# Optimization experiments

Hardware: AMD Instinct MI355X
Metric: run time of the kernel (lower is better)

Reference implementation:

```python
import jax, jax.numpy as jnp
import numpy as np

B, D, P, IEXT, T, H = 512, 64, 16, 8, 500, 128
DT = 1.0


def setup_inputs() -> dict:
    key = jax.random.key(0)
    ks = jax.random.split(key, 9)
    s = 0.01  # mimics normal(0.01) kernel init
    return {
        "x": jax.random.normal(ks[0], (B, D, T), jnp.float32),
        "p": jax.random.normal(ks[1], (B, P, T), jnp.float32),
        "i_ext": jax.random.normal(ks[2], (B, IEXT, T), jnp.float32),
        "W0": jax.random.normal(ks[3], (D + P, H), jnp.float32) * s,
        "b0": jax.random.normal(ks[4], (H,), jnp.float32) * s,
        "W1": jax.random.normal(ks[5], (H, H), jnp.float32) * s,
        "b1": jax.random.normal(ks[6], (H,), jnp.float32) * s,
        "W2": jax.random.normal(ks[7], (H, D), jnp.float32) * s,
        "b2": jax.random.normal(ks[8], (D,), jnp.float32) * s,
    }


def reference(x, p, i_ext, W0, b0, W1, b1, W2, b2):
    # Simple_MLP with extra_p=True: concat(state, p) -> Dense+tanh x2 -> Dense
    def mlp(z):
        z = jnp.tanh(z @ W0 + b0)
        z = jnp.tanh(z @ W1 + b1)
        return z @ W2 + b2

    def dfun(state, p_t):
        return mlp(jnp.concatenate([state, p_t], axis=-1))  # [B, D]

    # Heun step: predictor + corrector (two MLP evals), dt = 1.0
    def step(c, p_t):
        d1 = dfun(c, p_t)
        xi = c + DT * d1
        d2 = dfun(xi, p_t)
        nx = c + DT * 0.5 * (d1 + d2)
        return nx, c  # carry new state, emit previous state (as in Heun_step)

    x0 = x[..., 0]                    # [B, D] initial state
    p_seq = jnp.moveaxis(p, 2, 0)     # [T, B, P]
    # i_ext is scanned by the original module but never used by Simple_MLP.
    _, ys = jax.lax.scan(step, x0, p_seq)  # ys: [T, B, D]
    return jnp.moveaxis(ys, 0, 2)     # [B, D, T]
```

## Files before the change

### kernel.cpp

```cpp
#include <hip/hip_runtime.h>

namespace {

constexpr int kB = 512, kD = 64, kP = 16, kT = 500, kH = 128;
constexpr int kRows = 16;
constexpr int kBlocks = kB / kRows;
constexpr int kThreads = 256;

typedef __attribute__((ext_vector_type(8))) short short8;
typedef __attribute__((ext_vector_type(4))) float float4v;
typedef __attribute__((ext_vector_type(2))) unsigned int uint2v;

__device__ __forceinline__ float bf2f(unsigned short u) {
  union { unsigned int i; float f; } v;
  v.i = ((unsigned int)u) << 16;
  return v.f;
}
__device__ __forceinline__ unsigned short f2bf(float f) {
  union { float f; unsigned int i; } v;
  v.f = f;
  return (unsigned short)((v.i + 0x7FFFu + ((v.i >> 16) & 1u)) >> 16);
}
__device__ __forceinline__ void split_bf(float x, unsigned short& hi, unsigned short& lo) {
  hi = f2bf(x);
  lo = f2bf(x - bf2f(hi));
}
#if __has_builtin(__builtin_amdgcn_cvt_pk_bf16_f32)
__device__ __forceinline__ unsigned int pk_bf16(float a, float b) {
  auto v = __builtin_amdgcn_cvt_pk_bf16_f32(a, b);
  unsigned int u;
  __builtin_memcpy(&u, &v, 4);
  return u;
}
#else
__device__ __forceinline__ unsigned int pk_bf16(float a, float b) {
  return (unsigned int)f2bf(a) | ((unsigned int)f2bf(b) << 16);
}
#endif
__device__ __forceinline__ void sp2(float a, float b, unsigned int& hw, unsigned int& lw) {
  unsigned int uh = pk_bf16(a, b);
  float ah, bh;
  { unsigned int t1 = uh << 16; __builtin_memcpy(&ah, &t1, 4); }
  { unsigned int t2 = uh & 0xFFFF0000u; __builtin_memcpy(&bh, &t2, 4); }
  hw = uh;
  lw = pk_bf16(a - ah, b - bh);
}
__device__ __forceinline__ short8 mk8(unsigned int a, unsigned int b, unsigned int c,
                                      unsigned int d) {
  union { unsigned int w[4]; short8 s; } u;
  u.w[0] = a; u.w[1] = b; u.w[2] = c; u.w[3] = d;
  return u.s;
}
__device__ __forceinline__ float fast_tanh(float x) {
  float e = __builtin_amdgcn_exp2f(x * 2.885390081777927f);
  return 1.0f - 2.0f * __builtin_amdgcn_rcpf(e + 1.0f);
}

#define MFMA(a, b, c) __builtin_amdgcn_mfma_f32_16x16x32_bf16((a), (b), (c), 0, 0, 0)

__global__ __launch_bounds__(kThreads, 1) void node_kernel(
    const float* __restrict__ xg, const float* __restrict__ pg,
    const float* __restrict__ w0g, const float* __restrict__ b0g,
    const float* __restrict__ w1g, const float* __restrict__ b1g,
    const float* __restrict__ w2g, const float* __restrict__ b2g,
    float* __restrict__ outg) {
  __shared__ __align__(16) unsigned short h0p[16 * 128];
  __shared__ __align__(16) unsigned short h1p[16 * 128];
  __shared__ __align__(16) unsigned short zhp[16 * 64];
  __shared__ __align__(16) unsigned short zlp[16 * 64];

  const int tid = threadIdx.x;
  const int wv = tid >> 6;
  const int lane = tid & 63;
  const int l15 = lane & 15;
  const int q = lane >> 4;
  const int brow = blockIdx.x * kRows;
  const int sw = (l15 & 7) << 3;

  short8 wz[2][4], wp[2][2], w1f[2][8], w2f[8];
#pragma unroll
  for (int u = 0; u < 2; ++u) {
    const int T = 2 * wv + u;
    const int nW = 32 * (T >> 1) + 8 * (l15 >> 2) + 4 * (T & 1) + (l15 & 3);
#pragma unroll
    for (int kt = 0; kt < 2; ++kt) {
      short8 vh, vl;
#pragma unroll
      for (int j = 0; j < 8; ++j) {
        unsigned short hi, lo;
        split_bf(w0g[(kt * 32 + q * 8 + j) * kH + nW], hi, lo);
        vh[j] = (short)hi; vl[j] = (short)lo;
      }
      wz[u][kt] = vh; wz[u][2 + kt] = vl;
    }
    {
      short8 vh, vl;
#pragma unroll
      for (int j = 0; j < 8; ++j) {
        int k = 64 + q * 8 + j;
        unsigned short hi = 0, lo = 0;
        if (k < 80) split_bf(w0g[k * kH + nW], hi, lo);
        vh[j] = (short)hi; vl[j] = (short)lo;
      }
      wp[u][0] = vh; wp[u][1] = vl;
    }
#pragma unroll
    for (int kt = 0; kt < 4; ++kt) {
      short8 vh, vl;
#pragma unroll
      for (int j = 0; j < 8; ++j) {
        unsigned short hi, lo;
        split_bf(w1g[(kt * 32 + q * 8 + j) * kH + nW], hi, lo);
        vh[j] = (short)hi; vl[j] = (short)lo;
      }
      w1f[u][kt] = vh; w1f[u][4 + kt] = vl;
    }
  }
  {
    const int nW2 = 32 * (wv >> 1) + 8 * (l15 >> 2) + 4 * (wv & 1) + (l15 & 3);
#pragma unroll
    for (int kt = 0; kt < 4; ++kt) {
      short8 vh, vl;
#pragma unroll
      for (int j = 0; j < 8; ++j) {
        unsigned short hi, lo;
        split_bf(w2g[(kt * 32 + q * 8 + j) * kD + nW2], hi, lo);
        vh[j] = (short)hi; vl[j] = (short)lo;
      }
      w2f[kt] = vh; w2f[4 + kt] = vl;
    }
  }
#pragma unroll
  for (int u = 0; u < 2; ++u) {
    asm("" : "+a"(wz[u][0]), "+a"(wz[u][1]), "+a"(wz[u][2]), "+a"(wz[u][3]));
    asm("" : "+a"(wp[u][0]), "+a"(wp[u][1]));
    asm("" : "+a"(w1f[u][0]), "+a"(w1f[u][1]), "+a"(w1f[u][2]), "+a"(w1f[u][3]));
    asm("" : "+a"(w1f[u][4]), "+a"(w1f[u][5]), "+a"(w1f[u][6]), "+a"(w1f[u][7]));
  }
  asm("" : "+a"(w2f[0]), "+a"(w2f[1]), "+a"(w2f[2]), "+a"(w2f[3]));
  asm("" : "+a"(w2f[4]), "+a"(w2f[5]), "+a"(w2f[6]), "+a"(w2f[7]));

  const int bqw = 32 * wv + 8 * q;
  float4v b0v[2] = {*(const float4v*)&b0g[bqw], *(const float4v*)&b0g[bqw + 4]};
  float4v b1v[2] = {*(const float4v*)&b1g[bqw], *(const float4v*)&b1g[bqw + 4]};
  const int n0out = 32 * (wv >> 1) + 8 * q + 4 * (wv & 1);
  float4v b2v = *(const float4v*)&b2g[n0out];

  float stv[4];
#pragma unroll
  for (int r = 0; r < 4; ++r)
    stv[r] = xg[((size_t)(brow + l15) * kD + n0out + r) * kT];

  const float* prow = pg + ((size_t)(brow + l15) * kP + q * 8) * kT;
  float pcur[8];
#pragma unroll
  for (int j = 0; j < 8; ++j) pcur[j] = 0.f;
  if (q < 2) {
#pragma unroll
    for (int j = 0; j < 8; ++j) pcur[j] = prow[j * kT];
  }
  float* orow = outg + ((size_t)(brow + l15) * kD + n0out) * kT;

  const int zwi = l15 * 64 + (n0out ^ sw);
  const int hwi0 = l15 * 128 + ((bqw) ^ sw);
  const int hwi1 = l15 * 128 + ((bqw + 4) ^ sw);
#define RDH(plane, kt) (*(const short8*)&plane[l15 * 128 + ((((kt)*32) + q * 8) ^ sw)])
#define RDZ(plane, kt) (*(const short8*)&plane[l15 * 64 + ((((kt)*32) + q * 8) ^ sw)])

  {
    unsigned int hw0, lw0, hw1, lw1;
    sp2(stv[0], stv[1], hw0, lw0);
    sp2(stv[2], stv[3], hw1, lw1);
    *(uint2v*)&zhp[zwi] = (uint2v){hw0, hw1};
    *(uint2v*)&zlp[zwi] = (uint2v){lw0, lw1};
  }
  __syncthreads();

  const float4v Z4 = {0.f, 0.f, 0.f, 0.f};

  for (int t = 0; t < kT; ++t) {
    short8 zph, zpl;
    {
      unsigned int hw[4], lw[4];
#pragma unroll
      for (int u2 = 0; u2 < 4; ++u2) sp2(pcur[2 * u2], pcur[2 * u2 + 1], hw[u2], lw[u2]);
      zph = mk8(hw[0], hw[1], hw[2], hw[3]);
      zpl = mk8(lw[0], lw[1], lw[2], lw[3]);
    }
    float4v psum[2];
#pragma unroll
    for (int u = 0; u < 2; ++u) {
      float4v s = MFMA(wp[u][0], zph, b0v[u]);
      s = MFMA(wp[u][0], zpl, s);
      s = MFMA(wp[u][1], zph, s);
      psum[u] = s;
    }
    float pnx[8];
#pragma unroll
    for (int j = 0; j < 8; ++j) pnx[j] = 0.f;
    if (q < 2 && t + 1 < kT) {
#pragma unroll
      for (int j = 0; j < 8; ++j) pnx[j] = prow[j * kT + (t + 1)];
    }

    float d1v[4];
#pragma unroll
    for (int ev = 0; ev < 2; ++ev) {
      short8 zfh0 = RDZ(zhp, 0), zfh1 = RDZ(zhp, 1);
      short8 zfl0 = RDZ(zlp, 0), zfl1 = RDZ(zlp, 1);
#pragma unroll
      for (int u = 0; u < 2; ++u) {
        float4v acA = MFMA(wz[u][0], zfh0, psum[u]);
        acA = MFMA(wz[u][1], zfh1, acA);
        float4v acB = MFMA(wz[u][2], zfh0, Z4);
        acB = MFMA(wz[u][3], zfh1, acB);
        acB = MFMA(wz[u][0], zfl0, acB);
        acB = MFMA(wz[u][1], zfl1, acB);
        float4v a = acA + acB;
        unsigned int w0p2 = pk_bf16(fast_tanh(a[0]), fast_tanh(a[1]));
        unsigned int w1p2 = pk_bf16(fast_tanh(a[2]), fast_tanh(a[3]));
        *(uint2v*)&h0p[u ? hwi1 : hwi0] = (uint2v){w0p2, w1p2};
      }
      __syncthreads();
      short8 h0f0 = RDH(h0p, 0), h0f1 = RDH(h0p, 1);
      short8 h0f2 = RDH(h0p, 2), h0f3 = RDH(h0p, 3);
#pragma unroll
      for (int u = 0; u < 2; ++u) {
        float4v acA = MFMA(w1f[u][0], h0f0, b1v[u]);
        acA = MFMA(w1f[u][1], h0f1, acA);
        float4v acB = MFMA(w1f[u][2], h0f2, Z4);
        acB = MFMA(w1f[u][3], h0f3, acB);
        float4v acC = MFMA(w1f[u][4], h0f0, Z4);
        acC = MFMA(w1f[u][5], h0f1, acC);
        float4v acD = MFMA(w1f[u][6], h0f2, Z4);
        acD = MFMA(w1f[u][7], h0f3, acD);
        float4v a = (acA + acB) + (acC + acD);
        unsigned int w0p2 = pk_bf16(fast_tanh(a[0]), fast_tanh(a[1]));
        unsigned int w1p2 = pk_bf16(fast_tanh(a[2]), fast_tanh(a[3]));
        *(uint2v*)&h1p[u ? hwi1 : hwi0] = (uint2v){w0p2, w1p2};
      }
      __syncthreads();
      short8 h1f0 = RDH(h1p, 0), h1f1 = RDH(h1p, 1);
      short8 h1f2 = RDH(h1p, 2), h1f3 = RDH(h1p, 3);
      float4v acA = MFMA(w2f[0], h1f0, b2v);
      acA = MFMA(w2f[1], h1f1, acA);
      float4v acB = MFMA(w2f[2], h1f2, Z4);
      acB = MFMA(w2f[3], h1f3, acB);
      float4v acC = MFMA(w2f[4], h1f0, Z4);
      acC = MFMA(w2f[5], h1f1, acC);
      float4v acD = MFMA(w2f[6], h1f2, Z4);
      acD = MFMA(w2f[7], h1f3, acD);
      float4v a2v = (acA + acB) + (acC + acD);

      if (ev == 0) {
        float xi[4];
#pragma unroll
        for (int r = 0; r < 4; ++r) {
          d1v[r] = a2v[r];
          xi[r] = stv[r] + a2v[r];
        }
        unsigned int hw0, lw0, hw1, lw1;
        sp2(xi[0], xi[1], hw0, lw0);
        sp2(xi[2], xi[3], hw1, lw1);
        *(uint2v*)&zhp[zwi] = (uint2v){hw0, hw1};
        *(uint2v*)&zlp[zwi] = (uint2v){lw0, lw1};
      } else {
#pragma unroll
        for (int r = 0; r < 4; ++r) orow[r * kT + t] = stv[r];
#pragma unroll
        for (int r = 0; r < 4; ++r) stv[r] = stv[r] + 0.5f * (a2v[r] + d1v[r]);
        unsigned int hw0, lw0, hw1, lw1;
        sp2(stv[0], stv[1], hw0, lw0);
        sp2(stv[2], stv[3], hw1, lw1);
        *(uint2v*)&zhp[zwi] = (uint2v){hw0, hw1};
        *(uint2v*)&zlp[zwi] = (uint2v){lw0, lw1};
      }
      __syncthreads();
    }
#pragma unroll
    for (int j = 0; j < 8; ++j) pcur[j] = pnx[j];
  }
#undef RDH
#undef RDZ
}

}

extern "C" void kernel_launch(void* const* d_in, const int* in_sizes, int n_in,
                              void* d_out, int out_size, void* d_ws, size_t ws_size,
                              hipStream_t stream) {
  const float* xg = (const float*)d_in[0];
  const float* pg = (const float*)d_in[1];
  const float* w0g = (const float*)d_in[3];
  const float* b0g = (const float*)d_in[4];
  const float* w1g = (const float*)d_in[5];
  const float* b1g = (const float*)d_in[6];
  const float* w2g = (const float*)d_in[7];
  const float* b2g = (const float*)d_in[8];
  float* outg = (float*)d_out;

  hipLaunchKernelGGL(node_kernel, dim3(kBlocks), dim3(kThreads), 0, stream,
                     xg, pg, w0g, b0g, w1g, b1g, w2g, b2g, outg);
}
```

Baseline: 1.390 ms.

## Batch output stores via LDS staging and vectorize p prefetch in float4 chunks

Output states are staged in a shared-memory ring buffer over 8 timesteps, then flushed as coalesced float4 stores instead of scattered per-step scalar stores. The p inputs are loaded four timesteps at a time as float4 vectors and shifted in registers, so per-step scalar global loads go away. The p projection for the next step is computed early, inside the corrector phase, and MFMA accumulation chains are split for more ILP. This adds about 34KB of LDS and extra register pressure, and the tail flush relies on T mod 8 being 4.

```diff
diff --git a/kernel.cpp b/kernel.cpp
--- a/kernel.cpp
+++ b/kernel.cpp
@@ -68,6 +68,7 @@
   __shared__ __align__(16) unsigned short h1p[16 * 128];
   __shared__ __align__(16) unsigned short zhp[16 * 64];
   __shared__ __align__(16) unsigned short zlp[16 * 64];
+  __shared__ __align__(16) float yb[8][16 * 68];
 
   const int tid = threadIdx.x;
   const int wv = tid >> 6;
@@ -152,14 +153,14 @@
     stv[r] = xg[((size_t)(brow + l15) * kD + n0out + r) * kT];
 
   const float* prow = pg + ((size_t)(brow + l15) * kP + q * 8) * kT;
-  float pcur[8];
-#pragma unroll
-  for (int j = 0; j < 8; ++j) pcur[j] = 0.f;
+
+  float4v pq[8];
+#pragma unroll
+  for (int j = 0; j < 8; ++j) pq[j] = (float4v){0.f, 0.f, 0.f, 0.f};
   if (q < 2) {
 #pragma unroll
-    for (int j = 0; j < 8; ++j) pcur[j] = prow[j * kT];
-  }
-  float* orow = outg + ((size_t)(brow + l15) * kD + n0out) * kT;
+    for (int j = 0; j < 8; ++j) pq[j] = *(const float4v*)&prow[j * kT];
+  }
 
   const int zwi = l15 * 64 + (n0out ^ sw);
   const int hwi0 = l15 * 128 + ((bqw) ^ sw);
@@ -178,29 +179,50 @@
 
   const float4v Z4 = {0.f, 0.f, 0.f, 0.f};
 
+  auto calc_psum = [&](float4v* ps) {
+    unsigned int hw[4], lw[4];
+#pragma unroll
+    for (int u2 = 0; u2 < 4; ++u2) sp2(pq[2 * u2][0], pq[2 * u2 + 1][0], hw[u2], lw[u2]);
+    short8 zph = mk8(hw[0], hw[1], hw[2], hw[3]);
+    short8 zpl = mk8(lw[0], lw[1], lw[2], lw[3]);
+#pragma unroll
+    for (int u = 0; u < 2; ++u) {
+      float4v s1 = MFMA(wp[u][0], zph, b0v[u]);
+      float4v s2 = MFMA(wp[u][1], zph, Z4);
+      s2 = MFMA(wp[u][0], zpl, s2);
+      ps[u] = s1 + s2;
+    }
+  };
+  auto shiftpq = [&]() {
+#pragma unroll
+    for (int j = 0; j < 8; ++j) {
+      float4v t4 = pq[j];
+      pq[j] = (float4v){t4[1], t4[2], t4[3], t4[3]};
+    }
+  };
+
+  float4v psum[2];
+  calc_psum(psum);
+  shiftpq();
+
   for (int t = 0; t < kT; ++t) {
-    short8 zph, zpl;
-    {
-      unsigned int hw[4], lw[4];
-#pragma unroll
-      for (int u2 = 0; u2 < 4; ++u2) sp2(pcur[2 * u2], pcur[2 * u2 + 1], hw[u2], lw[u2]);
-      zph = mk8(hw[0], hw[1], hw[2], hw[3]);
-      zpl = mk8(lw[0], lw[1], lw[2], lw[3]);
-    }
-    float4v psum[2];
-#pragma unroll
-    for (int u = 0; u < 2; ++u) {
-      float4v s = MFMA(wp[u][0], zph, b0v[u]);
-      s = MFMA(wp[u][0], zpl, s);
-      s = MFMA(wp[u][1], zph, s);
-      psum[u] = s;
-    }
-    float pnx[8];
-#pragma unroll
-    for (int j = 0; j < 8; ++j) pnx[j] = 0.f;
-    if (q < 2 && t + 1 < kT) {
-#pragma unroll
-      for (int j = 0; j < 8; ++j) pnx[j] = prow[j * kT + (t + 1)];
+    if (((t & 3) == 3) && (t + 4 < kT) && q < 2) {
+#pragma unroll
+      for (int j = 0; j < 8; ++j) pq[j] = *(const float4v*)&prow[j * kT + t + 1];
+    }
+    if ((t & 7) == 0 && t) {
+      const int t0 = t - 8;
+#pragma unroll
+      for (int k2 = 0; k2 < 4; ++k2) {
+        int idx = tid + k2 * kThreads;
+        int rr = idx >> 6, cc = idx & 63;
+        float v[8];
+#pragma unroll
+        for (int s = 0; s < 8; ++s) v[s] = yb[s][rr * 68 + cc];
+        float* dst = outg + ((size_t)(brow + rr) * kD + cc) * kT + t0;
+        *(float4v*)dst = (float4v){v[0], v[1], v[2], v[3]};
+        *(float4v*)(dst + 4) = (float4v){v[4], v[5], v[6], v[7]};
+      }
     }
 
     float d1v[4];
@@ -214,9 +236,9 @@
         acA = MFMA(wz[u][1], zfh1, acA);
         float4v acB = MFMA(wz[u][2], zfh0, Z4);
         acB = MFMA(wz[u][3], zfh1, acB);
-        acB = MFMA(wz[u][0], zfl0, acB);
-        acB = MFMA(wz[u][1], zfl1, acB);
-        float4v a = acA + acB;
+        float4v acC = MFMA(wz[u][0], zfl0, Z4);
+        acC = MFMA(wz[u][1], zfl1, acC);
+        float4v a = acA + (acB + acC);
         unsigned int w0p2 = pk_bf16(fast_tanh(a[0]), fast_tanh(a[1]));
         unsigned int w1p2 = pk_bf16(fast_tanh(a[2]), fast_tanh(a[3]));
         *(uint2v*)&h0p[u ? hwi1 : hwi0] = (uint2v){w0p2, w1p2};
@@ -265,8 +287,12 @@
         *(uint2v*)&zhp[zwi] = (uint2v){hw0, hw1};
         *(uint2v*)&zlp[zwi] = (uint2v){lw0, lw1};
       } else {
-#pragma unroll
-        for (int r = 0; r < 4; ++r) orow[r * kT + t] = stv[r];
+        float4v psumN[2];
+        calc_psum(psumN);
+        shiftpq();
+#pragma unroll
+        for (int r = 0; r < 4; ++r)
+          yb[t & 7][l15 * 68 + n0out + r] = stv[r];
 #pragma unroll
         for (int r = 0; r < 4; ++r) stv[r] = stv[r] + 0.5f * (a2v[r] + d1v[r]);
         unsigned int hw0, lw0, hw1, lw1;
@@ -274,11 +300,25 @@
         sp2(stv[2], stv[3], hw1, lw1);
         *(uint2v*)&zhp[zwi] = (uint2v){hw0, hw1};
         *(uint2v*)&zlp[zwi] = (uint2v){lw0, lw1};
+        psum[0] = psumN[0];
+        psum[1] = psumN[1];
       }
       __syncthreads();
     }
-#pragma unroll
-    for (int j = 0; j < 8; ++j) pcur[j] = pnx[j];
+  }
+  __syncthreads();
+  {
+    const int t0 = (kT / 8) * 8;
+#pragma unroll
+    for (int k2 = 0; k2 < 4; ++k2) {
+      int idx = tid + k2 * kThreads;
+      int rr = idx >> 6, cc = idx & 63;
+      float v[4];
+#pragma unroll
+      for (int s = 0; s < 4; ++s) v[s] = yb[s][rr * 68 + cc];
+      float* dst = outg + ((size_t)(brow + rr) * kD + cc) * kT + t0;
+      *(float4v*)dst = (float4v){v[0], v[1], v[2], v[3]};
+    }
   }
 #undef RDH
 #undef RDZ
```

Measured after the change: 1.364 ms. About the same (-1.9%).
